# Kernel tuning notes

Hardware: AMD Instinct MI355X
Metric: run time of the kernel (lower is better)

## Reference

```python
import jax, jax.numpy as jnp
import numpy as np

B, IN, H = 8192, 2048, 2048


def setup_inputs() -> dict:
    key = jax.random.key(0)
    ks = jax.random.split(key, 8)
    s_in = 1.0 / np.sqrt(IN)
    s_h = 1.0 / np.sqrt(H)
    return {
        "x": jax.random.normal(ks[0], (B, IN), dtype=jnp.float32),
        "h": jax.random.normal(ks[1], (B, H), dtype=jnp.float32),
        "W_ir": jax.random.normal(ks[2], (H, IN), dtype=jnp.float32) * s_in,
        "b_ir": jnp.zeros((H,), dtype=jnp.float32),
        "W_hr": jax.random.normal(ks[3], (H, H), dtype=jnp.float32) * s_h,
        "W_iz": jax.random.normal(ks[4], (H, IN), dtype=jnp.float32) * s_in,
        "b_iz": jnp.zeros((H,), dtype=jnp.float32),
        "W_hz": jax.random.normal(ks[5], (H, H), dtype=jnp.float32) * s_h,
        "W_in": jax.random.normal(ks[6], (H, IN), dtype=jnp.float32) * s_in,
        "b_in": jnp.zeros((H,), dtype=jnp.float32),
        "W_hn": jax.random.normal(ks[7], (H, H), dtype=jnp.float32) * s_h,
    }


def reference(x, h, W_ir, b_ir, W_hr, W_iz, b_iz, W_hz, W_in, b_in, W_hn):
    # nn.Linear computes x @ W.T + b; weights stored [out, in].
    r = jax.nn.sigmoid(x @ W_ir.T + b_ir + h @ W_hr.T)
    z = jax.nn.sigmoid(x @ W_iz.T + b_iz + h @ W_hz.T)
    n = jnp.tanh(x @ W_in.T + b_in + (r * h) @ W_hn.T)
    h_t = (1.0 - z) * n + z * h
    return h_t, r, z, n
```

## Files before the change

kernel.cpp:

```cpp
#include <hip/hip_runtime.h>
#include <hip/hip_bf16.h>

#define B_DIM 8192
#define IN_DIM 2048
#define H_DIM 2048

#define BM 256
#define BN 256
#define BK 32
#define NT 128
#define NT_HALF 64
#define NBUF 4

typedef __attribute__((ext_vector_type(8))) short short8;
typedef __attribute__((ext_vector_type(4))) float f32x4;

__device__ __forceinline__ unsigned short f2bf(float f) {
    unsigned u = __builtin_bit_cast(unsigned, f);
    u += 0x7fffu + ((u >> 16) & 1u);
    return (unsigned short)(u >> 16);
}

__global__ void __launch_bounds__(256) cvt_f32_bf16(const float* __restrict__ in,
                                                    unsigned short* __restrict__ out,
                                                    int n8) {
    int i = blockIdx.x * blockDim.x + threadIdx.x;
    const int stride = gridDim.x * blockDim.x;
    for (; i < n8; i += stride) {
        const float4* p = (const float4*)in + (size_t)i * 2;
        float4 f0 = p[0], f1 = p[1];
        uint4 o;
        o.x = (unsigned)f2bf(f0.x) | ((unsigned)f2bf(f0.y) << 16);
        o.y = (unsigned)f2bf(f0.z) | ((unsigned)f2bf(f0.w) << 16);
        o.z = (unsigned)f2bf(f1.x) | ((unsigned)f2bf(f1.y) << 16);
        o.w = (unsigned)f2bf(f1.z) | ((unsigned)f2bf(f1.w) << 16);
        ((uint4*)out)[i] = o;
    }
}


#define STAGE(T, BUF)                                                          \
  do {                                                                         \
    const int _t = (T);                                                        \
    const unsigned short* _sa = (_t < NT_HALF) ? Asrc0 : Asrc1;                \
    const unsigned short* _sb = (_t < NT_HALF) ? Bsrc0 : Bsrc1;                \
    const int _k = (_t & (NT_HALF - 1)) * BK;                                  \
    char* _la = lds + (BUF) * 32768;                                           \
    __builtin_amdgcn_global_load_lds(                                          \
        (const __attribute__((address_space(1))) void*)                        \
            (_sa + (size_t)(brow + s_r) * 2048 + _k + s_co),                   \
        (__attribute__((address_space(3))) void*)(_la + tid * 16), 16, 0, 0);  \
    __builtin_amdgcn_global_load_lds(                                          \
        (const __attribute__((address_space(1))) void*)                        \
            (_sa + (size_t)(brow + s_r + 128) * 2048 + _k + s_co),             \
        (__attribute__((address_space(3))) void*)(_la + 8192 + tid * 16),      \
        16, 0, 0);                                                             \
    __builtin_amdgcn_global_load_lds(                                          \
        (const __attribute__((address_space(1))) void*)                        \
            (_sb + (size_t)(bcol + s_r) * 2048 + _k + s_co),                   \
        (__attribute__((address_space(3))) void*)(_la + 16384 + tid * 16),     \
        16, 0, 0);                                                             \
    __builtin_amdgcn_global_load_lds(                                          \
        (const __attribute__((address_space(1))) void*)                        \
            (_sb + (size_t)(bcol + s_r + 128) * 2048 + _k + s_co),             \
        (__attribute__((address_space(3))) void*)(_la + 24576 + tid * 16),     \
        16, 0, 0);                                                             \
  } while (0)

#define G_ITER(T, CUR, NXT, DO_STAGE, VMC)                                     \
  {                                                                            \
    if (DO_STAGE) { STAGE((T) + 2, ((T) + 2) & 3); }                           \
    asm volatile("s_waitcnt vmcnt(" VMC ")" ::: "memory");                     \
    __builtin_amdgcn_s_barrier();                                              \
    asm volatile("" ::: "memory");                                             \
    {                                                                          \
      const char* _pb = lds + ((T) & 3) * 32768;                               \
      _Pragma("unroll") for (int _nf = 0; _nf < 4; ++_nf)                      \
          fb[_nf] = *(const short8*)(_pb + offB[_nf]);                         \
    }                                                                          \
    if ((T) + 1 < NT) {                                                        \
      const char* _pa = lds + (((T) + 1) & 3) * 32768;                         \
      _Pragma("unroll") for (int _mf = 0; _mf < 8; ++_mf)                      \
          fa##NXT[_mf] = *(const short8*)(_pa + offA[_mf]);                    \
    }                                                                          \
    __builtin_amdgcn_s_setprio(1);                                             \
    _Pragma("unroll") for (int _mf = 0; _mf < 8; ++_mf)                        \
        _Pragma("unroll") for (int _nf = 0; _nf < 4; ++_nf)                    \
            acc[_mf][_nf] = __builtin_amdgcn_mfma_f32_16x16x32_bf16(           \
                fa##CUR[_mf], fb[_nf], acc[_mf][_nf], 0, 0, 0);                \
    __builtin_amdgcn_s_setprio(0);                                             \
  }

#define GEMM_CORE(A0P, B0P, A1P, B1P)                                          \
    __shared__ __align__(128) char lds[NBUF * 32768];                          \
    f32x4 acc[8][4] = {};                                                      \
    short8 fa0[8], fa1[8], fb[4];                                              \
    const int tid = threadIdx.x;                                               \
    const int wv = tid >> 6;                                                   \
    const int wm = wv >> 2, wn = wv & 3;                                       \
    const int fr = (tid & 63) & 15;                                            \
    const int fq = (tid & 63) >> 4;                                            \
    const int s_r = tid >> 2;                                                  \
    const int s_co = (((tid & 3) ^ ((s_r >> 1) & 3)) << 3);                    \
    const unsigned short* Asrc0 = (A0P);                                       \
    const unsigned short* Asrc1 = (A1P);                                       \
    const unsigned short* Bsrc0 = (B0P);                                       \
    const unsigned short* Bsrc1 = (B1P);                                       \
    int offA[8], offB[4];                                                      \
    _Pragma("unroll") for (int _i = 0; _i < 8; ++_i) {                         \
      const int _r = wm * 128 + _i * 16 + fr;                                  \
      offA[_i] = _r * 64 + ((fq ^ ((_r >> 1) & 3)) << 4);                      \
    }                                                                          \
    _Pragma("unroll") for (int _i = 0; _i < 4; ++_i) {                         \
      const int _r = wn * 64 + _i * 16 + fr;                                   \
      offB[_i] = 16384 + _r * 64 + ((fq ^ ((_r >> 1) & 3)) << 4);              \
    }                                                                          \
    STAGE(0, 0);                                                               \
    STAGE(1, 1);                                                               \
    asm volatile("s_waitcnt vmcnt(4)" ::: "memory");                           \
    __builtin_amdgcn_s_barrier();                                              \
    asm volatile("" ::: "memory");                                             \
    _Pragma("unroll") for (int _i = 0; _i < 8; ++_i)                           \
        fa0[_i] = *(const short8*)(lds + offA[_i]);                            \
    for (int t = 0; t < 124; t += 4) {                                         \
      G_ITER(t, 0, 1, 1, "4");                                                 \
      G_ITER(t + 1, 1, 0, 1, "4");                                             \
      G_ITER(t + 2, 0, 1, 1, "4");                                             \
      G_ITER(t + 3, 1, 0, 1, "4");                                             \
    }                                                                          \
    G_ITER(124, 0, 1, 1, "4");                                                 \
    G_ITER(125, 1, 0, 1, "4");                                                 \
    G_ITER(126, 0, 1, 0, "0");                                                 \
    G_ITER(127, 1, 0, 0, "0");

__global__ void __launch_bounds__(512, 2) gemm_rz(
    const unsigned short* __restrict__ xb, const unsigned short* __restrict__ hb,
    const unsigned short* __restrict__ Wir, const unsigned short* __restrict__ Whr,
    const unsigned short* __restrict__ Wiz, const unsigned short* __restrict__ Whz,
    const float* __restrict__ b_ir, const float* __restrict__ b_iz,
    const float* __restrict__ h_f32,
    float* __restrict__ out_r, float* __restrict__ out_z,
    unsigned short* __restrict__ rh)
{
    int bid = blockIdx.x;
    const int is_z = bid >= 256;
    if (is_z) bid -= 256;
    const int brow = (bid & 31) << 8;
    const int bcol = (bid >> 5) << 8;

    const unsigned short* Wi = is_z ? Wiz : Wir;
    const unsigned short* Wh = is_z ? Whz : Whr;

    GEMM_CORE(xb, Wi, hb, Wh)

    const float* bias = is_z ? b_iz : b_ir;
    float* outp = is_z ? out_z : out_r;

#pragma unroll
    for (int nf = 0; nf < 4; ++nf) {
        const int col = bcol + wn * 64 + nf * 16 + fr;
        const float bv = bias[col];
#pragma unroll
        for (int mf = 0; mf < 8; ++mf) {
            const int row0 = brow + wm * 128 + mf * 16 + fq * 4;
#pragma unroll
            for (int v = 0; v < 4; ++v) {
                const size_t idx = (size_t)(row0 + v) * 2048 + col;
                float s = acc[mf][nf][v] + bv;
                s = 1.0f / (1.0f + __expf(-s));
                outp[idx] = s;
                if (!is_z) rh[idx] = f2bf(s * h_f32[idx]);
            }
        }
    }
}

__global__ void __launch_bounds__(512, 2) gemm_n(
    const unsigned short* __restrict__ xb, const unsigned short* __restrict__ rh,
    const unsigned short* __restrict__ Win, const unsigned short* __restrict__ Whn,
    const float* __restrict__ b_in,
    const float* __restrict__ h_f32, const float* __restrict__ out_z,
    float* __restrict__ out_n, float* __restrict__ out_ht)
{
    const int bid = blockIdx.x;
    const int brow = (bid & 31) << 8;
    const int bcol = (bid >> 5) << 8;

    GEMM_CORE(xb, Win, rh, Whn)

#pragma unroll
    for (int nf = 0; nf < 4; ++nf) {
        const int col = bcol + wn * 64 + nf * 16 + fr;
        const float bv = b_in[col];
#pragma unroll
        for (int mf = 0; mf < 8; ++mf) {
            const int row0 = brow + wm * 128 + mf * 16 + fq * 4;
#pragma unroll
            for (int v = 0; v < 4; ++v) {
                const size_t idx = (size_t)(row0 + v) * 2048 + col;
                const float tn = tanhf(acc[mf][nf][v] + bv);
                out_n[idx] = tn;
                const float zv = out_z[idx];
                const float hv = h_f32[idx];
                out_ht[idx] = (1.0f - zv) * tn + zv * hv;
            }
        }
    }
}

extern "C" void kernel_launch(void* const* d_in, const int* in_sizes, int n_in,
                              void* d_out, int out_size, void* d_ws, size_t ws_size,
                              hipStream_t stream) {
    const float* x    = (const float*)d_in[0];
    const float* h    = (const float*)d_in[1];
    const float* W_ir = (const float*)d_in[2];
    const float* b_ir = (const float*)d_in[3];
    const float* W_hr = (const float*)d_in[4];
    const float* W_iz = (const float*)d_in[5];
    const float* b_iz = (const float*)d_in[6];
    const float* W_hz = (const float*)d_in[7];
    const float* W_in = (const float*)d_in[8];
    const float* b_in = (const float*)d_in[9];
    const float* W_hn = (const float*)d_in[10];

    const size_t NBH = (size_t)B_DIM * H_DIM;
    const size_t NW  = (size_t)H_DIM * IN_DIM;

    float* out_ht = (float*)d_out;
    float* out_r  = out_ht + NBH;
    float* out_z  = out_r + NBH;
    float* out_n  = out_z + NBH;

    unsigned short* ws   = (unsigned short*)d_ws;
    unsigned short* xb   = ws;
    unsigned short* hb   = xb + NBH;
    unsigned short* wirb = hb + NBH;
    unsigned short* whrb = wirb + NW;
    unsigned short* wizb = whrb + NW;
    unsigned short* whzb = wizb + NW;
    unsigned short* winb = whzb + NW;
    unsigned short* whnb = winb + NW;
    unsigned short* rh   = whnb + NW;

    const int CVT_BLOCKS = 2048;
    cvt_f32_bf16<<<CVT_BLOCKS, 256, 0, stream>>>(x, xb, (int)(NBH / 8));
    cvt_f32_bf16<<<CVT_BLOCKS, 256, 0, stream>>>(h, hb, (int)(NBH / 8));
    cvt_f32_bf16<<<CVT_BLOCKS, 256, 0, stream>>>(W_ir, wirb, (int)(NW / 8));
    cvt_f32_bf16<<<CVT_BLOCKS, 256, 0, stream>>>(W_hr, whrb, (int)(NW / 8));
    cvt_f32_bf16<<<CVT_BLOCKS, 256, 0, stream>>>(W_iz, wizb, (int)(NW / 8));
    cvt_f32_bf16<<<CVT_BLOCKS, 256, 0, stream>>>(W_hz, whzb, (int)(NW / 8));
    cvt_f32_bf16<<<CVT_BLOCKS, 256, 0, stream>>>(W_in, winb, (int)(NW / 8));
    cvt_f32_bf16<<<CVT_BLOCKS, 256, 0, stream>>>(W_hn, whnb, (int)(NW / 8));

    gemm_rz<<<512, 512, 0, stream>>>(xb, hb, wirb, whrb, wizb, whzb,
                                     b_ir, b_iz, h, out_r, out_z, rh);

    gemm_n<<<256, 512, 0, stream>>>(xb, rh, winb, whnb, b_in, h, out_z,
                                    out_n, out_ht);
}
```

Baseline: 1.024 ms.

## Restructure GEMM mainloop to BK=64 double-buffer with quadrant-split MFMA phases

Replaces the 4-buffer BK=32 pipeline with a 2-buffer BK=64 scheme that uses 128 KB of LDS. Each tile's compute is split into four quadrant phases, and a quarter of the next tile's global-to-LDS loads is issued in each phase, with barriers around the MFMA blocks. The swizzle changes to 8-way XOR for the wider rows. The aim is fewer barriers per K, larger MFMA batches and finer-grained load interleaving. The risks are that 128 KB LDS per block may limit occupancy, and that the added barriers may serialise the waves.

```diff
diff --git a/kernel.cpp b/kernel.cpp
--- a/kernel.cpp
+++ b/kernel.cpp
@@ -5,12 +5,7 @@
 #define IN_DIM 2048
 #define H_DIM 2048
 
-#define BM 256
-#define BN 256
-#define BK 32
-#define NT 128
-#define NT_HALF 64
-#define NBUF 4
+#define NTILE 32
 
 typedef __attribute__((ext_vector_type(8))) short short8;
 typedef __attribute__((ext_vector_type(4))) float f32x4;
@@ -39,99 +34,114 @@
 }
 
 
-#define STAGE(T, BUF)                                                          \
+#define BARRIER do { __builtin_amdgcn_s_barrier(); \
+                     asm volatile("" ::: "memory"); } while (0)
+
+#define STG_HALF(TT, H)                                                        \
   do {                                                                         \
-    const int _t = (T);                                                        \
-    const unsigned short* _sa = (_t < NT_HALF) ? Asrc0 : Asrc1;                \
-    const unsigned short* _sb = (_t < NT_HALF) ? Bsrc0 : Bsrc1;                \
-    const int _k = (_t & (NT_HALF - 1)) * BK;                                  \
-    char* _la = lds + (BUF) * 32768;                                           \
+    const int _t = (TT);                                                       \
+    const int _k = (_t & (NTILE - 1)) * 64;                                    \
+    const unsigned short* _src;                                                \
+    int _rbase;                                                                \
+    if ((H) < 2) { _src = (_t < NTILE) ? Asrc0 : Asrc1; _rbase = brow + (H) * 128; } \
+    else         { _src = (_t < NTILE) ? Bsrc0 : Bsrc1; _rbase = bcol + ((H) - 2) * 128; } \
+    char* _dst = lds + ((_t) & 1) * 65536 + (H) * 16384;                       \
     __builtin_amdgcn_global_load_lds(                                          \
         (const __attribute__((address_space(1))) void*)                        \
-            (_sa + (size_t)(brow + s_r) * 2048 + _k + s_co),                   \
-        (__attribute__((address_space(3))) void*)(_la + tid * 16), 16, 0, 0);  \
+            (_src + (size_t)(_rbase + s_r) * 2048 + _k + s_c),                 \
+        (__attribute__((address_space(3))) void*)(_dst + tid * 16), 16, 0, 0); \
     __builtin_amdgcn_global_load_lds(                                          \
         (const __attribute__((address_space(1))) void*)                        \
-            (_sa + (size_t)(brow + s_r + 128) * 2048 + _k + s_co),             \
-        (__attribute__((address_space(3))) void*)(_la + 8192 + tid * 16),      \
-        16, 0, 0);                                                             \
-    __builtin_amdgcn_global_load_lds(                                          \
-        (const __attribute__((address_space(1))) void*)                        \
-            (_sb + (size_t)(bcol + s_r) * 2048 + _k + s_co),                   \
-        (__attribute__((address_space(3))) void*)(_la + 16384 + tid * 16),     \
-        16, 0, 0);                                                             \
-    __builtin_amdgcn_global_load_lds(                                          \
-        (const __attribute__((address_space(1))) void*)                        \
-            (_sb + (size_t)(bcol + s_r + 128) * 2048 + _k + s_co),             \
-        (__attribute__((address_space(3))) void*)(_la + 24576 + tid * 16),     \
+            (_src + (size_t)(_rbase + 64 + s_r) * 2048 + _k + s_c),            \
+        (__attribute__((address_space(3))) void*)(_dst + 8192 + tid * 16),     \
         16, 0, 0);                                                             \
   } while (0)
 
-#define G_ITER(T, CUR, NXT, DO_STAGE, VMC)                                     \
+#define RD_A(DST, MH)                                                          \
+    _Pragma("unroll") for (int _mf = 0; _mf < 4; ++_mf)                        \
+      _Pragma("unroll") for (int _ks = 0; _ks < 2; ++_ks)                      \
+        DST[_mf * 2 + _ks] =                                                   \
+            *(const short8*)(bp + Abase + (MH) * 8192 + _mf * 2048 + cA[_ks]);
+
+#define RD_B(DST, NH)                                                          \
+    _Pragma("unroll") for (int _nf = 0; _nf < 2; ++_nf)                        \
+      _Pragma("unroll") for (int _ks = 0; _ks < 2; ++_ks)                      \
+        DST[_nf * 2 + _ks] =                                                   \
+            *(const short8*)(bp + Bbase + (NH) * 4096 + _nf * 2048 + cA[_ks]);
+
+#define QUAD(AM0, AN0, AFR, BFR)                                               \
+    _Pragma("unroll") for (int _mf = 0; _mf < 4; ++_mf)                        \
+      _Pragma("unroll") for (int _nf = 0; _nf < 2; ++_nf)                      \
+        _Pragma("unroll") for (int _ks = 0; _ks < 2; ++_ks)                    \
+          acc[(AM0) + _mf][(AN0) + _nf] =                                      \
+              __builtin_amdgcn_mfma_f32_16x16x32_bf16(                         \
+                  AFR[_mf * 2 + _ks], BFR[_nf * 2 + _ks],                      \
+                  acc[(AM0) + _mf][(AN0) + _nf], 0, 0, 0);
+
+#define TILE_BODY(T, S1, S2, S3, S4, WAITSTR)                                  \
   {                                                                            \
-    if (DO_STAGE) { STAGE((T) + 2, ((T) + 2) & 3); }                           \
-    asm volatile("s_waitcnt vmcnt(" VMC ")" ::: "memory");                     \
-    __builtin_amdgcn_s_barrier();                                              \
-    asm volatile("" ::: "memory");                                             \
-    {                                                                          \
-      const char* _pb = lds + ((T) & 3) * 32768;                               \
-      _Pragma("unroll") for (int _nf = 0; _nf < 4; ++_nf)                      \
-          fb[_nf] = *(const short8*)(_pb + offB[_nf]);                         \
-    }                                                                          \
-    if ((T) + 1 < NT) {                                                        \
-      const char* _pa = lds + (((T) + 1) & 3) * 32768;                         \
-      _Pragma("unroll") for (int _mf = 0; _mf < 8; ++_mf)                      \
-          fa##NXT[_mf] = *(const short8*)(_pa + offA[_mf]);                    \
-    }                                                                          \
-    __builtin_amdgcn_s_setprio(1);                                             \
-    _Pragma("unroll") for (int _mf = 0; _mf < 8; ++_mf)                        \
-        _Pragma("unroll") for (int _nf = 0; _nf < 4; ++_nf)                    \
-            acc[_mf][_nf] = __builtin_amdgcn_mfma_f32_16x16x32_bf16(           \
-                fa##CUR[_mf], fb[_nf], acc[_mf][_nf], 0, 0, 0);                \
-    __builtin_amdgcn_s_setprio(0);                                             \
+    const char* bp = lds + ((T) & 1) * 65536;                                  \
+    S1;                                                                        \
+    RD_A(a0, 0) RD_B(b0, 0)                                                    \
+    BARRIER;                                                                   \
+    __builtin_amdgcn_s_setprio(1);                                             \
+    QUAD(0, 0, a0, b0)                                                         \
+    __builtin_amdgcn_s_setprio(0);                                             \
+    BARRIER;                                                                   \
+    S2;                                                                        \
+    RD_B(b1, 1)                                                                \
+    BARRIER;                                                                   \
+    __builtin_amdgcn_s_setprio(1);                                             \
+    QUAD(0, 2, a0, b1)                                                         \
+    __builtin_amdgcn_s_setprio(0);                                             \
+    BARRIER;                                                                   \
+    S3;                                                                        \
+    RD_A(a1, 1)                                                                \
+    BARRIER;                                                                   \
+    __builtin_amdgcn_s_setprio(1);                                             \
+    QUAD(4, 0, a1, b0)                                                         \
+    __builtin_amdgcn_s_setprio(0);                                             \
+    BARRIER;                                                                   \
+    S4;                                                                        \
+    asm volatile("s_waitcnt vmcnt(" WAITSTR ")" ::: "memory");                 \
+    BARRIER;                                                                   \
+    __builtin_amdgcn_s_setprio(1);                                             \
+    QUAD(4, 2, a1, b1)                                                         \
+    __builtin_amdgcn_s_setprio(0);                                             \
+    BARRIER;                                                                   \
   }
 
 #define GEMM_CORE(A0P, B0P, A1P, B1P)                                          \
-    __shared__ __align__(128) char lds[NBUF * 32768];                          \
+    __shared__ __align__(128) char lds[131072];                                \
     f32x4 acc[8][4] = {};                                                      \
-    short8 fa0[8], fa1[8], fb[4];                                              \
+    short8 a0[8], a1[8], b0[4], b1[4];                                         \
     const int tid = threadIdx.x;                                               \
     const int wv = tid >> 6;                                                   \
     const int wm = wv >> 2, wn = wv & 3;                                       \
     const int fr = (tid & 63) & 15;                                            \
     const int fq = (tid & 63) >> 4;                                            \
-    const int s_r = tid >> 2;                                                  \
-    const int s_co = (((tid & 3) ^ ((s_r >> 1) & 3)) << 3);                    \
+    const int s_r = tid >> 3;                                       \
+    const int s_c = (((tid & 7) ^ (s_r & 7)) << 3);                \
     const unsigned short* Asrc0 = (A0P);                                       \
     const unsigned short* Asrc1 = (A1P);                                       \
     const unsigned short* Bsrc0 = (B0P);                                       \
     const unsigned short* Bsrc1 = (B1P);                                       \
-    int offA[8], offB[4];                                                      \
-    _Pragma("unroll") for (int _i = 0; _i < 8; ++_i) {                         \
-      const int _r = wm * 128 + _i * 16 + fr;                                  \
-      offA[_i] = _r * 64 + ((fq ^ ((_r >> 1) & 3)) << 4);                      \
+    const int Abase = (wm * 128 + fr) * 128;                                   \
+    const int Bbase = 32768 + (wn * 64 + fr) * 128;                            \
+    int cA[2];                                                                 \
+    cA[0] = ((fq ^ (fr & 7)) << 4);                                            \
+    cA[1] = (((4 + fq) ^ (fr & 7)) << 4);                                      \
+    STG_HALF(0, 0); STG_HALF(0, 1); STG_HALF(0, 2); STG_HALF(0, 3);            \
+    STG_HALF(1, 0);                                                            \
+    asm volatile("s_waitcnt vmcnt(2)" ::: "memory");                           \
+    BARRIER;                                                                   \
+    for (int t = 0; t < 62; ++t) {                                             \
+      TILE_BODY(t, STG_HALF(t + 1, 1), STG_HALF(t + 1, 2),                     \
+                STG_HALF(t + 1, 3), STG_HALF(t + 2, 0), "2")                   \
     }                                                                          \
-    _Pragma("unroll") for (int _i = 0; _i < 4; ++_i) {                         \
-      const int _r = wn * 64 + _i * 16 + fr;                                   \
-      offB[_i] = 16384 + _r * 64 + ((fq ^ ((_r >> 1) & 3)) << 4);              \
-    }                                                                          \
-    STAGE(0, 0);                                                               \
-    STAGE(1, 1);                                                               \
-    asm volatile("s_waitcnt vmcnt(4)" ::: "memory");                           \
-    __builtin_amdgcn_s_barrier();                                              \
-    asm volatile("" ::: "memory");                                             \
-    _Pragma("unroll") for (int _i = 0; _i < 8; ++_i)                           \
-        fa0[_i] = *(const short8*)(lds + offA[_i]);                            \
-    for (int t = 0; t < 124; t += 4) {                                         \
-      G_ITER(t, 0, 1, 1, "4");                                                 \
-      G_ITER(t + 1, 1, 0, 1, "4");                                             \
-      G_ITER(t + 2, 0, 1, 1, "4");                                             \
-      G_ITER(t + 3, 1, 0, 1, "4");                                             \
-    }                                                                          \
-    G_ITER(124, 0, 1, 1, "4");                                                 \
-    G_ITER(125, 1, 0, 1, "4");                                                 \
-    G_ITER(126, 0, 1, 0, "0");                                                 \
-    G_ITER(127, 1, 0, 0, "0");
+    TILE_BODY(62, STG_HALF(63, 1), STG_HALF(63, 2), STG_HALF(63, 3),           \
+              (void)0, "0")                                                    \
+    TILE_BODY(63, (void)0, (void)0, (void)0, (void)0, "0")
 
 __global__ void __launch_bounds__(512, 2) gemm_rz(
     const unsigned short* __restrict__ xb, const unsigned short* __restrict__ hb,
@@ -157,16 +167,16 @@
     float* outp = is_z ? out_z : out_r;
 
 #pragma unroll
-    for (int nf = 0; nf < 4; ++nf) {
-        const int col = bcol + wn * 64 + nf * 16 + fr;
+    for (int an = 0; an < 4; ++an) {
+        const int col = bcol + wn * 64 + an * 16 + fr;
         const float bv = bias[col];
 #pragma unroll
-        for (int mf = 0; mf < 8; ++mf) {
-            const int row0 = brow + wm * 128 + mf * 16 + fq * 4;
+        for (int am = 0; am < 8; ++am) {
+            const int row0 = brow + wm * 128 + am * 16 + fq * 4;
 #pragma unroll
             for (int v = 0; v < 4; ++v) {
                 const size_t idx = (size_t)(row0 + v) * 2048 + col;
-                float s = acc[mf][nf][v] + bv;
+                float s = acc[am][an][v] + bv;
                 s = 1.0f / (1.0f + __expf(-s));
                 outp[idx] = s;
                 if (!is_z) rh[idx] = f2bf(s * h_f32[idx]);
@@ -189,16 +199,16 @@
     GEMM_CORE(xb, Win, rh, Whn)
 
 #pragma unroll
-    for (int nf = 0; nf < 4; ++nf) {
-        const int col = bcol + wn * 64 + nf * 16 + fr;
+    for (int an = 0; an < 4; ++an) {
+        const int col = bcol + wn * 64 + an * 16 + fr;
         const float bv = b_in[col];
 #pragma unroll
-        for (int mf = 0; mf < 8; ++mf) {
-            const int row0 = brow + wm * 128 + mf * 16 + fq * 4;
+        for (int am = 0; am < 8; ++am) {
+            const int row0 = brow + wm * 128 + am * 16 + fq * 4;
 #pragma unroll
             for (int v = 0; v < 4; ++v) {
                 const size_t idx = (size_t)(row0 + v) * 2048 + col;
-                const float tn = tanhf(acc[mf][nf][v] + bv);
+                const float tn = tanhf(acc[am][an][v] + bv);
                 out_n[idx] = tn;
                 const float zv = out_z[idx];
                 const float hv = h_f32[idx];
```

Result: faster. 940.7 us (-8.1%).
